# Kernel tuning notes

Hardware: AMD Instinct MI355X
Metric: run time of the kernel (lower is better)

## Reference

```python
import jax, jax.numpy as jnp
import numpy as np

B, N, H, BD, P = 16, 128, 128, 64, 256

def setup_inputs() -> dict:
    key = jax.random.key(0)
    ks = jax.random.split(key, 10)
    s = lambda fan_in: 1.0 / np.sqrt(fan_in)
    return {
        "hidden_states": jax.random.normal(ks[0], (B, N, H), dtype=jnp.float32),
        "positions": jax.random.normal(ks[1], (B, N, 2), dtype=jnp.float32),
        "W1": jax.random.uniform(ks[2], (2, BD), jnp.float32, -s(2), s(2)),
        "b1": jax.random.uniform(ks[3], (BD,), jnp.float32, -s(2), s(2)),
        "W2": jax.random.uniform(ks[4], (H + BD, P), jnp.float32, -s(H + BD), s(H + BD)),
        "b2": jax.random.uniform(ks[5], (P,), jnp.float32, -s(H + BD), s(H + BD)),
        "W3": jax.random.uniform(ks[6], (P, P), jnp.float32, -s(P), s(P)),
        "b3": jax.random.uniform(ks[7], (P,), jnp.float32, -s(P), s(P)),
        "Wout": jax.random.uniform(ks[8], (P, P), jnp.float32, -s(P), s(P)),
        "bout": jax.random.uniform(ks[9], (P,), jnp.float32, -s(P), s(P)),
    }

def reference(hidden_states, positions, W1, b1, W2, b2, W3, b3, Wout, bout):
    b, n, h = hidden_states.shape
    # rel[b,i,j] = pos[b,j] - pos[b,i]  -> [B,N,N,2]
    rel = positions[:, None, :, :] - positions[:, :, None, :]
    enc = jax.nn.relu(rel @ W1 + b1)                       # [B,N,N,BD]
    hid = jnp.broadcast_to(hidden_states[:, None, :, :], (b, n, n, h))
    x = jnp.concatenate([hid, enc], axis=-1)               # [B,N,N,H+BD]
    emb = jax.nn.relu(x @ W2 + b2) @ W3 + b3               # [B,N,N,P]
    # mask self (j == i) with -inf before max-pool over neighbors j
    self_mask = jnp.eye(n, dtype=bool)[None, :, :, None]
    emb = jnp.where(self_mask, -jnp.inf, emb)
    pooled = emb.max(axis=2)                               # [B,N,P]
    return pooled @ Wout + bout
```

## Files before the change

### kernel.cpp

```cpp
#include <hip/hip_runtime.h>
#include <hip/hip_fp16.h>

using f16x4 = __attribute__((ext_vector_type(4))) _Float16;
using f16x8 = __attribute__((ext_vector_type(8))) _Float16;
using f32x4 = __attribute__((ext_vector_type(4))) float;
using f32x16 = __attribute__((ext_vector_type(16))) float;

__device__ __forceinline__ f16x4 ld_f16x4(const void* p) {
    return *reinterpret_cast<const f16x4*>(p);
}
__device__ __forceinline__ f16x8 ld_f16x8(const void* p) {
    return *reinterpret_cast<const f16x8*>(p);
}

__global__ void sp_wconv(const float* __restrict__ W2, const float* __restrict__ W3,
                         const float* __restrict__ pos, const float* __restrict__ W1,
                         const float* __restrict__ b1,
                         _Float16* __restrict__ W2bt, _Float16* __restrict__ W3s,
                         _Float16* __restrict__ T1h, _Float16* __restrict__ T1bh) {
    int t = blockIdx.x * 256 + threadIdx.x;
    if (t < 16384) {
        int p = t >> 6, k = t & 63;
        W2bt[t] = (_Float16)W2[(128 + k) * 256 + p];
    }
    {
        int kk = t >> 12, rem = t & 4095;
        int row = rem >> 4, inner = rem & 15;
        int slot = inner >> 3, e = inner & 7;
        int h = slot ^ ((row >> 2) & 1);
        int k = kk * 16 + (e & 3) + 8 * (e >> 2) + 4 * h;
        W3s[t] = (_Float16)W3[k * 256 + row];
    }
#pragma unroll
    for (int h = 0; h < 2; ++h) {
        int idx = t + h * 65536;
        int row = idx >> 6, k = idx & 63;
        float v = pos[row * 2] * W1[k] + pos[row * 2 + 1] * W1[64 + k];
        T1h[idx]  = (_Float16)v;
        T1bh[idx] = (_Float16)(v + b1[k]);
    }
}

__global__ void sp_hpart(const float* __restrict__ hs, const float* __restrict__ W2,
                         const float* __restrict__ b2, _Float16* __restrict__ hp16) {
    __shared__ float sh[8 * 128];
    int rb = blockIdx.x * 8;
    int tid = threadIdx.x;
    for (int t = tid; t < 1024; t += 256) sh[t] = hs[rb * 128 + t];
    __syncthreads();
    float acc[8];
    float bb = b2[tid];
#pragma unroll
    for (int r = 0; r < 8; ++r) acc[r] = bb;
    for (int k = 0; k < 128; ++k) {
        float w = W2[k * 256 + tid];
#pragma unroll
        for (int r = 0; r < 8; ++r) acc[r] += sh[r * 128 + k] * w;
    }
#pragma unroll
    for (int r = 0; r < 8; ++r) hp16[(rb + r) * 256 + tid] = (_Float16)acc[r];
}

__global__ __launch_bounds__(256, 2) void sp_main(
    const float* __restrict__ b3,
    const _Float16* __restrict__ hp16, const _Float16* __restrict__ W2bt,
    const _Float16* __restrict__ W3s, const _Float16* __restrict__ T1h,
    const _Float16* __restrict__ T1bh, float* __restrict__ pool) {
    __shared__ __align__(16) char sW3[16][4096];
    __shared__ _Float16 sPoolH[4][8][128];

    const int bid = blockIdx.x;
    const int ig = bid & 15, ph = (bid >> 4) & 1, b = bid >> 5;
    const int tid = threadIdx.x;
    const int wj = tid >> 6, lane = tid & 63;
    const int l31 = lane & 31, hi = lane >> 5;

    {
        const uint4* W3v = (const uint4*)W3s;
        uint4* dst = (uint4*)sW3;
#pragma unroll
        for (int c = 0; c < 16; ++c)
            dst[c * 256 + tid] = W3v[c * 512 + ph * 256 + tid];
    }

    const int jl = wj * 32 + l31;
    const _Float16* tjb = T1bh + (b * 128 + jl) * 64 + hi * 8;
    const _Float16* tib = T1h + (b * 128) * 64 + hi * 8;
    const _Float16* hpb = hp16 + (b * 128 + jl) * 256;
    const int slotB = (hi ^ ((l31 >> 2) & 1)) * 16;

    __syncthreads();

#pragma unroll 1
    for (int ii2 = 0; ii2 < 4; ++ii2) {
        const int i0 = ig * 8 + ii2 * 2;
        const int i1 = i0 + 1;

        const _Float16* w2p = W2bt;
        const _Float16* hpp = hpb;
        asm volatile("" : "+v"(w2p), "+v"(hpp));

        f16x8 benc[2][4];
#pragma unroll
        for (int s = 0; s < 4; ++s) {
            f16x8 tbv = ld_f16x8(tjb + s * 16);
            f16x8 cv0 = ld_f16x8(tib + i0 * 64 + s * 16);
            f16x8 cv1 = ld_f16x8(tib + i1 * 64 + s * 16);
#pragma unroll
            for (int e = 0; e < 8; ++e) {
                _Float16 d0 = tbv[e] - cv0[e];
                _Float16 d1 = tbv[e] - cv1[e];
                benc[0][s][e] = d0 > (_Float16)0 ? d0 : (_Float16)0;
                benc[1][s][e] = d1 > (_Float16)0 ? d1 : (_Float16)0;
            }
        }

        f32x16 eacc[2][4];
#pragma unroll
        for (int iq = 0; iq < 2; ++iq)
#pragma unroll
            for (int nt = 0; nt < 4; ++nt)
#pragma unroll
                for (int r = 0; r < 16; ++r) eacc[iq][nt][r] = 0.f;

#pragma unroll
        for (int t = 0; t < 8; ++t) {
            f32x16 a0, a1;
#pragma unroll
            for (int r = 0; r < 16; ++r) { a0[r] = 0.f; a1[r] = 0.f; }
#pragma unroll
            for (int s = 0; s < 4; ++s) {
                f16x8 aw = ld_f16x8(w2p + (t * 32 + l31) * 64 + s * 16 + hi * 8);
                a0 = __builtin_amdgcn_mfma_f32_32x32x16_f16(aw, benc[0][s], a0, 0, 0, 0);
                a1 = __builtin_amdgcn_mfma_f32_32x32x16_f16(aw, benc[1][s], a1, 0, 0, 0);
            }
            f16x4 hp0 = ld_f16x4(hpp + t * 32 + 4 * hi);
            f16x4 hp1 = ld_f16x4(hpp + t * 32 + 8 + 4 * hi);
            f16x4 hp2 = ld_f16x4(hpp + t * 32 + 16 + 4 * hi);
            f16x4 hp3 = ld_f16x4(hpp + t * 32 + 24 + 4 * hi);
            f16x8 u00, u01, u10, u11;
#pragma unroll
            for (int e = 0; e < 4; ++e) {
                _Float16 v;
                v = (_Float16)a0[e]      + hp0[e]; u00[e]     = v > (_Float16)0 ? v : (_Float16)0;
                v = (_Float16)a0[e + 4]  + hp1[e]; u00[e + 4] = v > (_Float16)0 ? v : (_Float16)0;
                v = (_Float16)a0[e + 8]  + hp2[e]; u01[e]     = v > (_Float16)0 ? v : (_Float16)0;
                v = (_Float16)a0[e + 12] + hp3[e]; u01[e + 4] = v > (_Float16)0 ? v : (_Float16)0;
                v = (_Float16)a1[e]      + hp0[e]; u10[e]     = v > (_Float16)0 ? v : (_Float16)0;
                v = (_Float16)a1[e + 4]  + hp1[e]; u10[e + 4] = v > (_Float16)0 ? v : (_Float16)0;
                v = (_Float16)a1[e + 8]  + hp2[e]; u11[e]     = v > (_Float16)0 ? v : (_Float16)0;
                v = (_Float16)a1[e + 12] + hp3[e]; u11[e + 4] = v > (_Float16)0 ? v : (_Float16)0;
            }
#pragma unroll
            for (int nt = 0; nt < 4; ++nt) {
                const char* rowp = (const char*)sW3 + (nt * 32 + l31) * 32 + slotB;
                f16x8 bf0 = ld_f16x8(rowp + (2 * t) * 4096);
                f16x8 bf1 = ld_f16x8(rowp + (2 * t + 1) * 4096);
                eacc[0][nt] = __builtin_amdgcn_mfma_f32_32x32x16_f16(u00, bf0, eacc[0][nt], 0, 0, 0);
                eacc[1][nt] = __builtin_amdgcn_mfma_f32_32x32x16_f16(u10, bf0, eacc[1][nt], 0, 0, 0);
                eacc[0][nt] = __builtin_amdgcn_mfma_f32_32x32x16_f16(u01, bf1, eacc[0][nt], 0, 0, 0);
                eacc[1][nt] = __builtin_amdgcn_mfma_f32_32x32x16_f16(u11, bf1, eacc[1][nt], 0, 0, 0);
            }
        }

#pragma unroll
        for (int iq = 0; iq < 2; ++iq) {
            const int i = iq ? i1 : i0;
#pragma unroll
            for (int nt = 0; nt < 4; ++nt) {
                float m = -INFINITY;
#pragma unroll
                for (int r = 0; r < 16; ++r) {
                    int jrow = wj * 32 + (r & 3) + 8 * (r >> 2) + 4 * hi;
                    float v = eacc[iq][nt][r];
                    if (jrow != i) m = fmaxf(m, v);
                }
                m = fmaxf(m, __shfl_xor(m, 32));
                if (lane < 32) sPoolH[wj][ii2 * 2 + iq][nt * 32 + l31] = (_Float16)m;
            }
        }
    }
    __syncthreads();

#pragma unroll
    for (int q = 0; q < 4; ++q) {
        int idx = q * 256 + tid;
        int ii = idx >> 7, t = idx & 127;
        float v = fmaxf(fmaxf((float)sPoolH[0][ii][t], (float)sPoolH[1][ii][t]),
                        fmaxf((float)sPoolH[2][ii][t], (float)sPoolH[3][ii][t]));
        int p = ph * 128 + t;
        pool[(b * 128 + ig * 8 + ii) * 256 + p] = v + b3[p];
    }
}

__global__ void sp_out(const float* __restrict__ Wout, const float* __restrict__ bout,
                       float* __restrict__ io) {
    __shared__ float sp[8 * 256];
    int rb = blockIdx.x * 8;
    int tid = threadIdx.x;
    for (int t = tid; t < 2048; t += 256) sp[t] = io[rb * 256 + t];
    __syncthreads();
    float acc[8];
    float bb = bout[tid];
#pragma unroll
    for (int r = 0; r < 8; ++r) acc[r] = bb;
    for (int k = 0; k < 256; ++k) {
        float w = Wout[k * 256 + tid];
#pragma unroll
        for (int r = 0; r < 8; ++r) acc[r] += sp[r * 256 + k] * w;
    }
#pragma unroll
    for (int r = 0; r < 8; ++r) io[(rb + r) * 256 + tid] = acc[r];
}

extern "C" void kernel_launch(void* const* d_in, const int* in_sizes, int n_in,
                              void* d_out, int out_size, void* d_ws, size_t ws_size,
                              hipStream_t stream) {
    const float* hs   = (const float*)d_in[0];
    const float* pos  = (const float*)d_in[1];
    const float* W1   = (const float*)d_in[2];
    const float* b1   = (const float*)d_in[3];
    const float* W2   = (const float*)d_in[4];
    const float* b2   = (const float*)d_in[5];
    const float* W3   = (const float*)d_in[6];
    const float* b3   = (const float*)d_in[7];
    const float* Wout = (const float*)d_in[8];
    const float* bout = (const float*)d_in[9];
    float* out = (float*)d_out;

    _Float16* hp16 = (_Float16*)d_ws;
    _Float16* W2bt = (_Float16*)((char*)d_ws + (1 << 20));
    _Float16* W3s  = (_Float16*)((char*)d_ws + (1 << 20) + 32768);
    _Float16* T1h  = (_Float16*)((char*)d_ws + (1 << 20) + 32768 + 131072);
    _Float16* T1bh = (_Float16*)((char*)d_ws + (1 << 20) + 32768 + 131072 + 262144);

    sp_wconv<<<256, 256, 0, stream>>>(W2, W3, pos, W1, b1, W2bt, W3s, T1h, T1bh);
    sp_hpart<<<256, 256, 0, stream>>>(hs, W2, b2, hp16);
    sp_main<<<512, 256, 0, stream>>>(b3, hp16, W2bt, W3s, T1h, T1bh, out);
    sp_out<<<256, 256, 0, stream>>>(Wout, bout, out);
}
```

Before: 94.91 us.

## Fuse prep kernels, prefetch permuted hidden partials, use nontemporal loads, split out GEMM

Merges the weight-conversion and hidden-projection kernels into one launch, removing a kernel boundary. The hidden-projection output is written in a permuted layout so the main kernel can read it as two 8-wide vectors and prefetch the next tile's values one iteration ahead. Several global loads become nontemporal. The final output GEMM uses 4 rows per block over 512 blocks instead of 8 over 256, for more parallelism at the cost of more repeated Wout reads.

```diff
diff --git a/kernel.cpp b/kernel.cpp
--- a/kernel.cpp
+++ b/kernel.cpp
@@ -5,20 +5,28 @@
 using f16x8 = __attribute__((ext_vector_type(8))) _Float16;
 using f32x4 = __attribute__((ext_vector_type(4))) float;
 using f32x16 = __attribute__((ext_vector_type(16))) float;
-
-__device__ __forceinline__ f16x4 ld_f16x4(const void* p) {
-    return *reinterpret_cast<const f16x4*>(p);
-}
+using u32x4 = __attribute__((ext_vector_type(4))) unsigned int;
+
 __device__ __forceinline__ f16x8 ld_f16x8(const void* p) {
     return *reinterpret_cast<const f16x8*>(p);
 }
-
-__global__ void sp_wconv(const float* __restrict__ W2, const float* __restrict__ W3,
-                         const float* __restrict__ pos, const float* __restrict__ W1,
-                         const float* __restrict__ b1,
-                         _Float16* __restrict__ W2bt, _Float16* __restrict__ W3s,
-                         _Float16* __restrict__ T1h, _Float16* __restrict__ T1bh) {
-    int t = blockIdx.x * 256 + threadIdx.x;
+__device__ __forceinline__ f16x8 ldnt_f16x8(const void* p) {
+    return __builtin_nontemporal_load(reinterpret_cast<const f16x8*>(p));
+}
+__device__ __forceinline__ u32x4 ldnt_u4(const void* p) {
+    return __builtin_nontemporal_load(reinterpret_cast<const u32x4*>(p));
+}
+
+__global__ void sp_prep(const float* __restrict__ W2, const float* __restrict__ W3,
+                        const float* __restrict__ pos, const float* __restrict__ W1,
+                        const float* __restrict__ b1, const float* __restrict__ hs,
+                        const float* __restrict__ b2,
+                        _Float16* __restrict__ W2bt, _Float16* __restrict__ W3s,
+                        _Float16* __restrict__ T1h, _Float16* __restrict__ T1bh,
+                        _Float16* __restrict__ hp16) {
+    __shared__ float sh[8 * 128];
+    const int tid = threadIdx.x;
+    const int t = blockIdx.x * 256 + tid;
     if (t < 16384) {
         int p = t >> 6, k = t & 63;
         W2bt[t] = (_Float16)W2[(128 + k) * 256 + p];
@@ -39,14 +47,8 @@
         T1h[idx]  = (_Float16)v;
         T1bh[idx] = (_Float16)(v + b1[k]);
     }
-}
-
-__global__ void sp_hpart(const float* __restrict__ hs, const float* __restrict__ W2,
-                         const float* __restrict__ b2, _Float16* __restrict__ hp16) {
-    __shared__ float sh[8 * 128];
-    int rb = blockIdx.x * 8;
-    int tid = threadIdx.x;
-    for (int t = tid; t < 1024; t += 256) sh[t] = hs[rb * 128 + t];
+    const int rb = blockIdx.x * 8;
+    for (int q = tid; q < 1024; q += 256) sh[q] = hs[rb * 128 + q];
     __syncthreads();
     float acc[8];
     float bb = b2[tid];
@@ -57,8 +59,11 @@
 #pragma unroll
         for (int r = 0; r < 8; ++r) acc[r] += sh[r * 128 + k] * w;
     }
-#pragma unroll
-    for (int r = 0; r < 8; ++r) hp16[(rb + r) * 256 + tid] = (_Float16)acc[r];
+    int tt = tid >> 5, rem = tid & 31;
+    int q = rem >> 3, hi = (rem >> 2) & 1, rr = tid & 3;
+    int widx = tt * 32 + hi * 16 + q * 4 + rr;
+#pragma unroll
+    for (int r = 0; r < 8; ++r) hp16[(rb + r) * 256 + widx] = (_Float16)acc[r];
 }
 
 __global__ __launch_bounds__(256, 2) void sp_main(
@@ -76,11 +81,11 @@
     const int l31 = lane & 31, hi = lane >> 5;
 
     {
-        const uint4* W3v = (const uint4*)W3s;
-        uint4* dst = (uint4*)sW3;
+        const u32x4* W3v = (const u32x4*)W3s;
+        u32x4* dst = (u32x4*)sW3;
 #pragma unroll
         for (int c = 0; c < 16; ++c)
-            dst[c * 256 + tid] = W3v[c * 512 + ph * 256 + tid];
+            dst[c * 256 + tid] = ldnt_u4(W3v + c * 512 + ph * 256 + tid);
     }
 
     const int jl = wj * 32 + l31;
@@ -100,12 +105,15 @@
         const _Float16* hpp = hpb;
         asm volatile("" : "+v"(w2p), "+v"(hpp));
 
+        f16x8 hpA_c = ldnt_f16x8(hpp + hi * 16);
+        f16x8 hpB_c = ldnt_f16x8(hpp + hi * 16 + 8);
+
         f16x8 benc[2][4];
 #pragma unroll
         for (int s = 0; s < 4; ++s) {
-            f16x8 tbv = ld_f16x8(tjb + s * 16);
-            f16x8 cv0 = ld_f16x8(tib + i0 * 64 + s * 16);
-            f16x8 cv1 = ld_f16x8(tib + i1 * 64 + s * 16);
+            f16x8 tbv = ldnt_f16x8(tjb + s * 16);
+            f16x8 cv0 = ldnt_f16x8(tib + i0 * 64 + s * 16);
+            f16x8 cv1 = ldnt_f16x8(tib + i1 * 64 + s * 16);
 #pragma unroll
             for (int e = 0; e < 8; ++e) {
                 _Float16 d0 = tbv[e] - cv0[e];
@@ -134,22 +142,23 @@
                 a0 = __builtin_amdgcn_mfma_f32_32x32x16_f16(aw, benc[0][s], a0, 0, 0, 0);
                 a1 = __builtin_amdgcn_mfma_f32_32x32x16_f16(aw, benc[1][s], a1, 0, 0, 0);
             }
-            f16x4 hp0 = ld_f16x4(hpp + t * 32 + 4 * hi);
-            f16x4 hp1 = ld_f16x4(hpp + t * 32 + 8 + 4 * hi);
-            f16x4 hp2 = ld_f16x4(hpp + t * 32 + 16 + 4 * hi);
-            f16x4 hp3 = ld_f16x4(hpp + t * 32 + 24 + 4 * hi);
+            f16x8 hpA_n = hpA_c, hpB_n = hpB_c;
+            if (t < 7) {
+                hpA_n = ldnt_f16x8(hpp + (t + 1) * 32 + hi * 16);
+                hpB_n = ldnt_f16x8(hpp + (t + 1) * 32 + hi * 16 + 8);
+            }
             f16x8 u00, u01, u10, u11;
 #pragma unroll
             for (int e = 0; e < 4; ++e) {
                 _Float16 v;
-                v = (_Float16)a0[e]      + hp0[e]; u00[e]     = v > (_Float16)0 ? v : (_Float16)0;
-                v = (_Float16)a0[e + 4]  + hp1[e]; u00[e + 4] = v > (_Float16)0 ? v : (_Float16)0;
-                v = (_Float16)a0[e + 8]  + hp2[e]; u01[e]     = v > (_Float16)0 ? v : (_Float16)0;
-                v = (_Float16)a0[e + 12] + hp3[e]; u01[e + 4] = v > (_Float16)0 ? v : (_Float16)0;
-                v = (_Float16)a1[e]      + hp0[e]; u10[e]     = v > (_Float16)0 ? v : (_Float16)0;
-                v = (_Float16)a1[e + 4]  + hp1[e]; u10[e + 4] = v > (_Float16)0 ? v : (_Float16)0;
-                v = (_Float16)a1[e + 8]  + hp2[e]; u11[e]     = v > (_Float16)0 ? v : (_Float16)0;
-                v = (_Float16)a1[e + 12] + hp3[e]; u11[e + 4] = v > (_Float16)0 ? v : (_Float16)0;
+                v = (_Float16)a0[e]      + hpA_c[e];     u00[e]     = v > (_Float16)0 ? v : (_Float16)0;
+                v = (_Float16)a0[e + 4]  + hpA_c[e + 4]; u00[e + 4] = v > (_Float16)0 ? v : (_Float16)0;
+                v = (_Float16)a0[e + 8]  + hpB_c[e];     u01[e]     = v > (_Float16)0 ? v : (_Float16)0;
+                v = (_Float16)a0[e + 12] + hpB_c[e + 4]; u01[e + 4] = v > (_Float16)0 ? v : (_Float16)0;
+                v = (_Float16)a1[e]      + hpA_c[e];     u10[e]     = v > (_Float16)0 ? v : (_Float16)0;
+                v = (_Float16)a1[e + 4]  + hpA_c[e + 4]; u10[e + 4] = v > (_Float16)0 ? v : (_Float16)0;
+                v = (_Float16)a1[e + 8]  + hpB_c[e];     u11[e]     = v > (_Float16)0 ? v : (_Float16)0;
+                v = (_Float16)a1[e + 12] + hpB_c[e + 4]; u11[e + 4] = v > (_Float16)0 ? v : (_Float16)0;
             }
 #pragma unroll
             for (int nt = 0; nt < 4; ++nt) {
@@ -161,6 +170,8 @@
                 eacc[0][nt] = __builtin_amdgcn_mfma_f32_32x32x16_f16(u01, bf1, eacc[0][nt], 0, 0, 0);
                 eacc[1][nt] = __builtin_amdgcn_mfma_f32_32x32x16_f16(u11, bf1, eacc[1][nt], 0, 0, 0);
             }
+            hpA_c = hpA_n;
+            hpB_c = hpB_n;
         }
 
 #pragma unroll
@@ -195,22 +206,22 @@
 
 __global__ void sp_out(const float* __restrict__ Wout, const float* __restrict__ bout,
                        float* __restrict__ io) {
-    __shared__ float sp[8 * 256];
-    int rb = blockIdx.x * 8;
+    __shared__ float sp[4 * 256];
+    int rb = blockIdx.x * 4;
     int tid = threadIdx.x;
-    for (int t = tid; t < 2048; t += 256) sp[t] = io[rb * 256 + t];
-    __syncthreads();
-    float acc[8];
+    for (int t = tid; t < 1024; t += 256) sp[t] = io[rb * 256 + t];
+    __syncthreads();
+    float acc[4];
     float bb = bout[tid];
 #pragma unroll
-    for (int r = 0; r < 8; ++r) acc[r] = bb;
+    for (int r = 0; r < 4; ++r) acc[r] = bb;
     for (int k = 0; k < 256; ++k) {
         float w = Wout[k * 256 + tid];
 #pragma unroll
-        for (int r = 0; r < 8; ++r) acc[r] += sp[r * 256 + k] * w;
-    }
-#pragma unroll
-    for (int r = 0; r < 8; ++r) io[(rb + r) * 256 + tid] = acc[r];
+        for (int r = 0; r < 4; ++r) acc[r] += sp[r * 256 + k] * w;
+    }
+#pragma unroll
+    for (int r = 0; r < 4; ++r) io[(rb + r) * 256 + tid] = acc[r];
 }
 
 extern "C" void kernel_launch(void* const* d_in, const int* in_sizes, int n_in,
@@ -234,8 +245,8 @@
     _Float16* T1h  = (_Float16*)((char*)d_ws + (1 << 20) + 32768 + 131072);
     _Float16* T1bh = (_Float16*)((char*)d_ws + (1 << 20) + 32768 + 131072 + 262144);
 
-    sp_wconv<<<256, 256, 0, stream>>>(W2, W3, pos, W1, b1, W2bt, W3s, T1h, T1bh);
-    sp_hpart<<<256, 256, 0, stream>>>(hs, W2, b2, hp16);
+    sp_prep<<<256, 256, 0, stream>>>(W2, W3, pos, W1, b1, hs, b2,
+                                     W2bt, W3s, T1h, T1bh, hp16);
     sp_main<<<512, 256, 0, stream>>>(b3, hp16, W2bt, W3s, T1h, T1bh, out);
-    sp_out<<<256, 256, 0, stream>>>(Wout, bout, out);
-}
+    sp_out<<<512, 256, 0, stream>>>(Wout, bout, out);
+}
```

After: 83.54 us. 1.14x faster.
